# Optimization experiments

Measured on AMD Instinct MI355X. Metric: run time of the kernel, lower is better.

The kernel has to match this reference:

```python
import jax, jax.numpy as jnp
import numpy as np

D, U, NNZ, B = 8192, 4096, 1_700_000, 1024

def setup_inputs() -> dict:
    key = jax.random.key(0)
    k1, k2, k3, k4 = jax.random.split(key, 4)
    x = jax.random.normal(k1, (B, D), dtype=jnp.float32)
    kernel_vector = jax.random.normal(k2, (NNZ,), dtype=jnp.float32) * 0.02
    bias = jax.random.normal(k3, (U,), dtype=jnp.float32) * 0.01
    flat = jax.random.randint(k4, (NNZ,), 0, D * U)  # random sparsity pattern
    nonzero_ind = jnp.stack([flat // U, flat % U], axis=1).astype(jnp.int32)  # [NNZ, 2]
    return {"x": x, "kernel_vector": kernel_vector, "bias": bias, "nonzero_ind": nonzero_ind}

def reference(x, kernel_vector, bias, nonzero_ind):
    # scatter_nd: build dense (D, U) kernel from nonzero entries (duplicates add, as in tf.scatter_nd)
    W = jnp.zeros((D, U), dtype=kernel_vector.dtype).at[nonzero_ind[:, 0], nonzero_ind[:, 1]].add(kernel_vector)
    out = x @ W + bias  # [B, U]
    return jnp.tanh(out)
```

## Files before the change

### kernel.cpp

```cpp
#include <hip/hip_runtime.h>
#include <hip/hip_fp16.h>
#include <cmath>

#define DIM_M 1024
#define DIM_K 8192
#define DIM_N 4096
#define SPLIT 4
#define KSPL  (DIM_K / SPLIT)
#define BKT   64
#define NT    (KSPL / BKT)
#define NB    1024
#define EPB   8192

typedef __attribute__((ext_vector_type(8))) _Float16 half8;
typedef __attribute__((ext_vector_type(4))) float floatx4;

struct __align__(8) Half4 { __half2 a, b; };

__device__ inline void gload_lds16(const void* g, void* l) {
    __builtin_amdgcn_global_load_lds(
        (const __attribute__((address_space(1))) void*)g,
        (__attribute__((address_space(3))) void*)l, 16, 0, 0);
}

__global__ void cvt_f2h(const floatx4* __restrict__ in, Half4* __restrict__ out, int n4) {
    int i = blockIdx.x * blockDim.x + threadIdx.x;
    if (i < n4) {
        floatx4 f = in[i];
        Half4 h;
        h.a = __floats2half2_rn(f.x, f.y);
        h.b = __floats2half2_rn(f.z, f.w);
        out[i] = h;
    }
}


__global__ __launch_bounds__(512) void hist_k(const int* __restrict__ ind,
                                              unsigned* __restrict__ cnt, int nnz) {
    __shared__ unsigned h[NB];
    const int tid = threadIdx.x;
    for (int i = tid; i < NB; i += 512) h[i] = 0u;
    __syncthreads();
    const int base = blockIdx.x * EPB;
    const int lim = min(nnz - base, EPB);
    const int4* ip = (const int4*)(ind + 2 * (size_t)base);
    for (int k2 = tid; k2 < lim / 2; k2 += 512) {
        int4 w = ip[k2];
        atomicAdd(&h[w.y >> 2], 1u);
        atomicAdd(&h[w.w >> 2], 1u);
    }
    if ((lim & 1) && tid == 0) {
        int u = ind[2 * (size_t)(base + lim - 1) + 1];
        atomicAdd(&h[u >> 2], 1u);
    }
    __syncthreads();
    for (int i = tid; i < NB; i += 512) cnt[(size_t)blockIdx.x * NB + i] = h[i];
}

__global__ void scanb_k(unsigned* cnt, unsigned* __restrict__ bb, int nblk) {
    __shared__ unsigned s[256];
    const int tid = threadIdx.x, bin = blockIdx.x;
    unsigned carry = 0;
    for (int c0 = 0; c0 < nblk; c0 += 256) {
        int b = c0 + tid;
        unsigned v = (b < nblk) ? cnt[(size_t)b * NB + bin] : 0u;
        s[tid] = v;
        __syncthreads();
        for (int off = 1; off < 256; off <<= 1) {
            unsigned add = (tid >= off) ? s[tid - off] : 0u;
            __syncthreads();
            s[tid] += add;
            __syncthreads();
        }
        if (b < nblk) cnt[(size_t)b * NB + bin] = carry + s[tid] - v;
        carry += s[255];
        __syncthreads();
    }
    if (tid == 0) bb[bin] = carry;
}

__global__ void scant_k(unsigned* bb) {
    __shared__ unsigned s[NB];
    const int tid = threadIdx.x;
    unsigned v = bb[tid];
    s[tid] = v;
    __syncthreads();
    for (int off = 1; off < NB; off <<= 1) {
        unsigned add = (tid >= off) ? s[tid - off] : 0u;
        __syncthreads();
        s[tid] += add;
        __syncthreads();
    }
    bb[tid] = s[tid] - v;
    if (tid == NB - 1) bb[NB] = s[tid];
}

__global__ __launch_bounds__(512) void reorder_k(const int* __restrict__ ind,
                                                 const float* __restrict__ kv,
                                                 const unsigned* __restrict__ start,
                                                 const unsigned* __restrict__ bb,
                                                 uint2* __restrict__ ebuf, int nnz) {
    extern __shared__ char rsm[];
    uint2*    buf  = (uint2*)rsm;
    unsigned* gofs = (unsigned*)(rsm + 65536);
    unsigned* cur  = (unsigned*)(rsm + 98304);
    unsigned* dl   = (unsigned*)(rsm + 102400);
    unsigned* ss   = (unsigned*)(rsm + 106496);
    const int tid = threadIdx.x, blk = blockIdx.x;
    const int base = blk * EPB;
    const int lim = min(nnz - base, EPB);
    const int4*   ip = (const int4*)(ind + 2 * (size_t)base);
    const float2* vp = (const float2*)(kv + base);

    for (int i = tid; i < NB; i += 512) cur[i] = 0u;
    __syncthreads();
    for (int k2 = tid; k2 < lim / 2; k2 += 512) {
        int4 w = ip[k2];
        atomicAdd(&cur[w.y >> 2], 1u);
        atomicAdd(&cur[w.w >> 2], 1u);
    }
    if ((lim & 1) && tid == 0) {
        int u = ind[2 * (size_t)(base + lim - 1) + 1];
        atomicAdd(&cur[u >> 2], 1u);
    }
    __syncthreads();
    unsigned c0 = cur[2 * tid], c1 = cur[2 * tid + 1];
    unsigned own = c0 + c1;
    ss[tid] = own;
    __syncthreads();
    for (int off = 1; off < 512; off <<= 1) {
        unsigned t = (tid >= off) ? ss[tid - off] : 0u;
        __syncthreads();
        ss[tid] += t;
        __syncthreads();
    }
    unsigned e0 = ss[tid] - own;
    unsigned e1 = e0 + c0;
    __syncthreads();
    cur[2 * tid]     = e0;
    cur[2 * tid + 1] = e1;
    unsigned g0 = bb[2 * tid]     + start[(size_t)blk * NB + 2 * tid];
    unsigned g1 = bb[2 * tid + 1] + start[(size_t)blk * NB + 2 * tid + 1];
    dl[2 * tid]     = g0 - e0;
    dl[2 * tid + 1] = g1 - e1;
    __syncthreads();
    for (int k2 = tid; k2 < lim / 2; k2 += 512) {
        int4 w = ip[k2];
        float2 v = vp[k2];
        int b0 = w.y >> 2, b1 = w.w >> 2;
        unsigned r0 = atomicAdd(&cur[b0], 1u);
        buf[r0]  = make_uint2(((unsigned)(w.y & 3) << 13) | (unsigned)w.x, __float_as_uint(v.x));
        gofs[r0] = dl[b0] + r0;
        unsigned r1 = atomicAdd(&cur[b1], 1u);
        buf[r1]  = make_uint2(((unsigned)(w.w & 3) << 13) | (unsigned)w.z, __float_as_uint(v.y));
        gofs[r1] = dl[b1] + r1;
    }
    if ((lim & 1) && tid == 0) {
        size_t e = (size_t)base + lim - 1;
        int d = ind[2 * e], u = ind[2 * e + 1];
        int b = u >> 2;
        unsigned r = atomicAdd(&cur[b], 1u);
        buf[r]  = make_uint2(((unsigned)(u & 3) << 13) | (unsigned)d, __float_as_uint(kv[e]));
        gofs[r] = dl[b] + r;
    }
    __syncthreads();
    for (int j = tid; j < lim; j += 512)
        ebuf[gofs[j]] = buf[j];
}

__global__ __launch_bounds__(512) void accum_k(const uint2* __restrict__ ebuf,
                                               const unsigned* __restrict__ bb,
                                               Half4* __restrict__ wh4) {
    extern __shared__ float reg[];
    floatx4* reg4 = (floatx4*)reg;
    const int tid = threadIdx.x, bin = blockIdx.x;
    for (int i = tid; i < 8192; i += 512) reg4[i] = floatx4{0.f, 0.f, 0.f, 0.f};
    __syncthreads();
    const unsigned s0 = bb[bin], s1 = bb[bin + 1];
    for (unsigned e = s0 + tid; e < s1; e += 512) {
        uint2 p = ebuf[e];
        atomicAdd(&reg[p.x], __uint_as_float(p.y));
    }
    __syncthreads();
    for (int i = tid; i < 8192; i += 512) {
        floatx4 f = reg4[i];
        Half4 h;
        h.a = __floats2half2_rn(f.x, f.y);
        h.b = __floats2half2_rn(f.z, f.w);
        wh4[(size_t)bin * 8192 + i] = h;
    }
}

__global__ __launch_bounds__(1024, 4) void gemm8_k(
    const _Float16* __restrict__ Ah,
    const _Float16* __restrict__ Bh,
    float*          __restrict__ part)
{
    extern __shared__ char smem[];

    const int tid  = threadIdx.x;
    const int lane = tid & 63;
    const int wave = tid >> 6;

    const int bid = blockIdx.x;
    const int swz = (bid & 7) * 32 + (bid >> 3);
    const int n0  = (swz >> 4) * 256;
    const int rem = swz & 15;
    const int m0  = (rem >> 2) * 256;
    const int sp  = rem & 3;
    const size_t kbase = (size_t)sp * KSPL;

    const int srow = tid >> 3;
    const int sch  = (tid & 7) ^ (srow & 7);
    const _Float16* aSg = Ah + (size_t)(m0 + srow) * DIM_K + kbase + sch * 8;
    const _Float16* bSg = Bh + (size_t)(n0 + srow) * DIM_K + kbase + sch * 8;
    char* aLg = smem + wave * 1024;
    char* bLg = smem + 32768 + wave * 1024;

    const int wn  = wave & 3;
    const int wrm = wave >> 2;
    const int q   = lane >> 4;
    const int l7  = lane & 7;
    const char* aRd = smem + (wrm * 64 + (lane & 15)) * 128;
    const char* bRd = smem + 32768 + (wn * 64 + (lane & 15)) * 128;
    const int ch0 = ((0 * 4 + q) ^ l7) * 16;
    const int ch1 = ((1 * 4 + q) ^ l7) * 16;

    floatx4 acc[4][4] = {};
    half8 aF[4], bF[4];

#define STAGE(C)                                                              \
    { _Pragma("unroll") for (int p = 0; p < 2; ++p) {                         \
        gload_lds16(aSg + (size_t)p * (128 * DIM_K), aLg + (C) * 65536 + p * 16384); \
        gload_lds16(bSg + (size_t)p * (128 * DIM_K), bLg + (C) * 65536 + p * 16384); } \
      aSg += BKT; bSg += BKT; }

#define PH(C, CH)                                                             \
    { _Pragma("unroll") for (int i = 0; i < 4; ++i)                           \
        aF[i] = *(const half8*)(aRd + (C) * 65536 + i * 2048 + (CH));         \
      _Pragma("unroll") for (int i = 0; i < 4; ++i)                           \
        bF[i] = *(const half8*)(bRd + (C) * 65536 + i * 2048 + (CH));         \
      asm volatile("s_waitcnt lgkmcnt(0)" ::: "memory");                      \
      __builtin_amdgcn_sched_barrier(0);                                      \
      __builtin_amdgcn_s_setprio(1);                                          \
      _Pragma("unroll") for (int mi = 0; mi < 4; ++mi)                        \
        _Pragma("unroll") for (int ni = 0; ni < 4; ++ni)                      \
          acc[mi][ni] = __builtin_amdgcn_mfma_f32_16x16x32_f16(               \
              aF[mi], bF[ni], acc[mi][ni], 0, 0, 0);                          \
      __builtin_amdgcn_s_setprio(0); }

#define KTILE(C) PH(C, ch0) PH(C, ch1)

    STAGE(0)
    STAGE(1)
    asm volatile("s_waitcnt vmcnt(4)" ::: "memory");
    __builtin_amdgcn_s_barrier();

    for (int t2 = 0; t2 < NT / 2; ++t2) {
        KTILE(0)
        __builtin_amdgcn_s_barrier();
        if (t2 < NT / 2 - 1) {
            STAGE(0)
            asm volatile("s_waitcnt vmcnt(4)" ::: "memory");
        } else {
            asm volatile("s_waitcnt vmcnt(0)" ::: "memory");
        }
        __builtin_amdgcn_s_barrier();
        KTILE(1)
        if (t2 < NT / 2 - 1) {
            __builtin_amdgcn_s_barrier();
            STAGE(1)
            asm volatile("s_waitcnt vmcnt(4)" ::: "memory");
            __builtin_amdgcn_s_barrier();
        }
    }

#undef KTILE
#undef PH
#undef STAGE

    float* pbase = part + (size_t)sp * DIM_M * DIM_N;
    #pragma unroll
    for (int ni = 0; ni < 4; ++ni) {
        const int col = n0 + wn * 64 + ni * 16 + (lane & 15);
        #pragma unroll
        for (int mi = 0; mi < 4; ++mi) {
            const int row = m0 + wrm * 64 + mi * 16 + (q << 2);
            #pragma unroll
            for (int r = 0; r < 4; ++r)
                pbase[(size_t)(row + r) * DIM_N + col] = acc[mi][ni][r];
        }
    }
}

__global__ void reduce_tanh(const floatx4* __restrict__ part, const float* __restrict__ bias,
                            floatx4* __restrict__ out) {
    const int n4 = DIM_M * DIM_N / 4;
    int i = blockIdx.x * blockDim.x + threadIdx.x;
    if (i < n4) {
        floatx4 s = part[i];
        #pragma unroll
        for (int sp = 1; sp < SPLIT; ++sp)
            s += part[(size_t)sp * n4 + i];
        floatx4 b = ((const floatx4*)bias)[i & (DIM_N / 4 - 1)];
        floatx4 o;
        o.x = tanhf(s.x + b.x);
        o.y = tanhf(s.y + b.y);
        o.z = tanhf(s.z + b.z);
        o.w = tanhf(s.w + b.w);
        out[i] = o;
    }
}

extern "C" void kernel_launch(void* const* d_in, const int* in_sizes, int n_in,
                              void* d_out, int out_size, void* d_ws, size_t ws_size,
                              hipStream_t stream) {
    const float* x    = (const float*)d_in[0];
    const float* kv   = (const float*)d_in[1];
    const float* bias = (const float*)d_in[2];
    const int*   ind  = (const int*)d_in[3];
    float* out = (float*)d_out;
    const int nnz = in_sizes[1];

    char* ws = (char*)d_ws;
    _Float16* wh = (_Float16*)ws;
    const size_t whBytes = (size_t)DIM_N * DIM_K * 2;
    _Float16* xh = (_Float16*)(ws + whBytes);
    const size_t xhBytes = (size_t)DIM_M * DIM_K * 2;
    float* part = (float*)(ws + whBytes + xhBytes);
    const size_t partBytes = (size_t)SPLIT * DIM_M * DIM_N * 4;
    uint2* ebuf = (uint2*)(ws + whBytes + xhBytes + partBytes);
    const size_t ebufBytes = (size_t)16 << 20;
    unsigned* cnt = (unsigned*)(ws + whBytes + xhBytes + partBytes + ebufBytes);
    const size_t cntBytes = (size_t)1024 * NB * 4;
    unsigned* bb = (unsigned*)(ws + whBytes + xhBytes + partBytes + ebufBytes + cntBytes);

    const int xN4 = (int)((size_t)DIM_M * DIM_K / 4);
    const int oN4 = DIM_M * DIM_N / 4;
    const int nblk = (nnz + EPB - 1) / EPB;

    cvt_f2h<<<(xN4 + 255) / 256, 256, 0, stream>>>((const floatx4*)x, (Half4*)xh, xN4);
    hist_k<<<nblk, 512, 0, stream>>>(ind, cnt, nnz);
    scanb_k<<<NB, 256, 0, stream>>>(cnt, bb, nblk);
    scant_k<<<1, NB, 0, stream>>>(bb);

    hipFuncSetAttribute((const void*)reorder_k,
                        hipFuncAttributeMaxDynamicSharedMemorySize, 131072);
    reorder_k<<<nblk, 512, 110592, stream>>>(ind, kv, cnt, bb, ebuf, nnz);

    hipFuncSetAttribute((const void*)accum_k,
                        hipFuncAttributeMaxDynamicSharedMemorySize, 131072);
    accum_k<<<NB, 512, 131072, stream>>>(ebuf, bb, (Half4*)wh);

    hipFuncSetAttribute((const void*)gemm8_k,
                        hipFuncAttributeMaxDynamicSharedMemorySize, 131072);
    gemm8_k<<<dim3(256), 1024, 131072, stream>>>(xh, wh, part);

    reduce_tanh<<<(oN4 + 255) / 256, 256, 0, stream>>>((const floatx4*)part, bias, (floatx4*)out);
}
```

Before: 138.7 us.

## Store split-K partials in fp16 and stagger LDS chunk order across waves

The GEMM now writes its split-K partial sums as fp16 instead of fp32, and the reduce kernel reads them back as fp16. This halves the partial-buffer traffic on both the write and the read side. Odd and even waves also process the two K-chunks of each tile in swapped order, which is meant to reduce LDS bank conflicts between waves. Rounding the partials to fp16 adds precision error before the summation and tanh.

```diff
diff --git a/kernel.cpp b/kernel.cpp
--- a/kernel.cpp
+++ b/kernel.cpp
@@ -194,7 +194,7 @@
 __global__ __launch_bounds__(1024, 4) void gemm8_k(
     const _Float16* __restrict__ Ah,
     const _Float16* __restrict__ Bh,
-    float*          __restrict__ part)
+    _Float16*       __restrict__ part)
 {
     extern __shared__ char smem[];
 
@@ -225,6 +225,8 @@
     const char* bRd = smem + 32768 + (wn * 64 + (lane & 15)) * 128;
     const int ch0 = ((0 * 4 + q) ^ l7) * 16;
     const int ch1 = ((1 * 4 + q) ^ l7) * 16;
+    const int chA = (wave & 1) ? ch1 : ch0;
+    const int chB = (wave & 1) ? ch0 : ch1;
 
     floatx4 acc[4][4] = {};
     half8 aF[4], bF[4];
@@ -249,7 +251,7 @@
               aF[mi], bF[ni], acc[mi][ni], 0, 0, 0);                          \
       __builtin_amdgcn_s_setprio(0); }
 
-#define KTILE(C) PH(C, ch0) PH(C, ch1)
+#define KTILE(C) PH(C, chA) PH(C, chB)
 
     STAGE(0)
     STAGE(1)
@@ -279,7 +281,7 @@
 #undef PH
 #undef STAGE
 
-    float* pbase = part + (size_t)sp * DIM_M * DIM_N;
+    _Float16* pbase = part + (size_t)sp * DIM_M * DIM_N;
     #pragma unroll
     for (int ni = 0; ni < 4; ++ni) {
         const int col = n0 + wn * 64 + ni * 16 + (lane & 15);
@@ -288,26 +290,30 @@
             const int row = m0 + wrm * 64 + mi * 16 + (q << 2);
             #pragma unroll
             for (int r = 0; r < 4; ++r)
-                pbase[(size_t)(row + r) * DIM_N + col] = acc[mi][ni][r];
-        }
-    }
-}
-
-__global__ void reduce_tanh(const floatx4* __restrict__ part, const float* __restrict__ bias,
+                pbase[(size_t)(row + r) * DIM_N + col] = (_Float16)acc[mi][ni][r];
+        }
+    }
+}
+
+__global__ void reduce_tanh(const Half4* __restrict__ part, const float* __restrict__ bias,
                             floatx4* __restrict__ out) {
     const int n4 = DIM_M * DIM_N / 4;
     int i = blockIdx.x * blockDim.x + threadIdx.x;
     if (i < n4) {
-        floatx4 s = part[i];
+        float sx = 0.f, sy = 0.f, sz = 0.f, sw = 0.f;
         #pragma unroll
-        for (int sp = 1; sp < SPLIT; ++sp)
-            s += part[(size_t)sp * n4 + i];
+        for (int sp = 0; sp < SPLIT; ++sp) {
+            Half4 p = part[(size_t)sp * n4 + i];
+            float2 lo = __half22float2(p.a);
+            float2 hi = __half22float2(p.b);
+            sx += lo.x; sy += lo.y; sz += hi.x; sw += hi.y;
+        }
         floatx4 b = ((const floatx4*)bias)[i & (DIM_N / 4 - 1)];
         floatx4 o;
-        o.x = tanhf(s.x + b.x);
-        o.y = tanhf(s.y + b.y);
-        o.z = tanhf(s.z + b.z);
-        o.w = tanhf(s.w + b.w);
+        o.x = tanhf(sx + b.x);
+        o.y = tanhf(sy + b.y);
+        o.z = tanhf(sz + b.z);
+        o.w = tanhf(sw + b.w);
         out[i] = o;
     }
 }
@@ -327,8 +333,8 @@
     const size_t whBytes = (size_t)DIM_N * DIM_K * 2;
     _Float16* xh = (_Float16*)(ws + whBytes);
     const size_t xhBytes = (size_t)DIM_M * DIM_K * 2;
-    float* part = (float*)(ws + whBytes + xhBytes);
-    const size_t partBytes = (size_t)SPLIT * DIM_M * DIM_N * 4;
+    _Float16* part = (_Float16*)(ws + whBytes + xhBytes);
+    const size_t partBytes = (size_t)SPLIT * DIM_M * DIM_N * 2;
     uint2* ebuf = (uint2*)(ws + whBytes + xhBytes + partBytes);
     const size_t ebufBytes = (size_t)16 << 20;
     unsigned* cnt = (unsigned*)(ws + whBytes + xhBytes + partBytes + ebufBytes);
@@ -356,5 +362,5 @@
                         hipFuncAttributeMaxDynamicSharedMemorySize, 131072);
     gemm8_k<<<dim3(256), 1024, 131072, stream>>>(xh, wh, part);
 
-    reduce_tanh<<<(oN4 + 255) / 256, 256, 0, stream>>>((const floatx4*)part, bias, (floatx4*)out);
-}
+    reduce_tanh<<<(oN4 + 255) / 256, 256, 0, stream>>>((const Half4*)part, bias, (floatx4*)out);
+}
```

New measurement: 131.8 us. 5.0% less time.
